# Kernel optimization log

Hardware: AMD Instinct MI355X
Metric: run time of the kernel (lower is better)

Reference implementation:

```python
import jax, jax.numpy as jnp
import numpy as np

B, N, D1, D2, H = 1, 1024, 128, 64, 4
C = D1 // H
PQ = PV = 4
DHALF = D2 // 2


def _ln(x, g, b):
    m = jnp.mean(x, -1, keepdims=True)
    v = jnp.var(x, -1, keepdims=True)
    return (x - m) / jnp.sqrt(v + 1e-5) * g + b


def _ipa(x, R, t, wq, wk, wv, wqp, wkp, wvp, headw, wout, bout):
    # AlphaFold2-style Invariant Point Attention (no pair bias: none is passed).
    q = (x @ wq).reshape(B, N, H, C)
    k = (x @ wk).reshape(B, N, H, C)
    v = (x @ wv).reshape(B, N, H, C)
    qp = (x @ wqp).reshape(B, N, H, PQ, 3)
    kp = (x @ wkp).reshape(B, N, H, PQ, 3)
    vp = (x @ wvp).reshape(B, N, H, PV, 3)
    to_glob = lambda p: jnp.einsum('bnij,bnhpj->bnhpi', R, p) + t[:, :, None, None, :]
    qpg, kpg, vpg = to_glob(qp), to_glob(kp), to_glob(vp)
    scalar = jnp.einsum('bihc,bjhc->bhij', q, k) / np.sqrt(C).astype(np.float32)
    # squared point distances via expansion (avoids B,N,N,H,P,3 intermediate)
    qq = jnp.sum(qpg ** 2, axis=(-1, -2))  # (B,N,H)
    kk = jnp.sum(kpg ** 2, axis=(-1, -2))
    qk = jnp.einsum('bihpx,bjhpx->bhij', qpg, kpg)
    d2 = qq.transpose(0, 2, 1)[:, :, :, None] + kk.transpose(0, 2, 1)[:, :, None, :] - 2.0 * qk
    gamma = jax.nn.softplus(headw)  # (H,)
    wC = np.float32(np.sqrt(2.0 / (9.0 * PQ)))
    wL = np.float32(np.sqrt(0.5))  # two logit terms
    logits = wL * (scalar - gamma[None, :, None, None] * (wC * 0.5) * d2)
    att = jax.nn.softmax(logits, axis=-1)  # (B,H,N,N)
    o = jnp.einsum('bhij,bjhc->bihc', att, v).reshape(B, N, H * C)
    opt = jnp.einsum('bhij,bjhpx->bihpx', att, vpg)  # global output points
    opt_l = jnp.einsum('bnji,bnhpj->bnhpi', R, opt - t[:, :, None, None, :])  # back to local frame
    norms = jnp.sqrt(jnp.sum(opt_l ** 2, -1) + 1e-8)  # (B,N,H,PV)
    feat = jnp.concatenate([o, opt_l.reshape(B, N, H * PV * 3), norms.reshape(B, N, H * PV)], -1)
    return feat @ wout + bout


def _forward(seq_1d, pair_2d, frames_R, frames_t,
             ln1_g, ln1_b, w_qkv, b_qkv, w_o, b_o, w_2to1, b_2to1,
             lnff_g, lnff_b, w_ff1, b_ff1, w_ff2, b_ff2,
             w_l, b_l, w_r, b_r, w_conv, b_conv,
             ipa_wq, ipa_wk, ipa_wv, ipa_wqp, ipa_wkp, ipa_wvp,
             ipa_headw, ipa_wout, ipa_bout, ln3_g, ln3_b):
    # --- 1D track: pre-LN MHA ---
    res = seq_1d
    xn = _ln(seq_1d, ln1_g, ln1_b)
    qkv = xn @ w_qkv + b_qkv  # (B,N,3*D1)
    q, k, v = jnp.split(qkv, 3, axis=-1)
    q = q.reshape(B, N, H, C); k = k.reshape(B, N, H, C); v = v.reshape(B, N, H, C)
    att = jax.nn.softmax(jnp.einsum('bihc,bjhc->bhij', q, k) / np.sqrt(C).astype(np.float32), -1)
    a = jnp.einsum('bhij,bjhc->bihc', att, v).reshape(B, N, D1) @ w_o + b_o
    x = res + a  # dropout is identity in eval
    # --- pair -> 1D aggregation (mean over j of INPUT pair) ---
    x = x + pair_2d.mean(axis=2) @ w_2to1 + b_2to1
    # --- FFN ---
    hdn = _ln(x, lnff_g, lnff_b)
    x = x + jax.nn.gelu(hdn @ w_ff1 + b_ff1, approximate=False) @ w_ff2 + b_ff2
    # --- 1D -> pair outer(-sum) update, zero-padded to D2 channels ---
    left = x @ w_l + b_l    # (B,N,D2//2)
    right = x @ w_r + b_r
    outer = left[:, :, None, :] + right[:, None, :, :]  # (B,N,N,D2//2)
    pair = pair_2d + jnp.pad(outer, ((0, 0), (0, 0), (0, 0), (0, D2 - DHALF)))
    # --- 1x1 conv on pair == per-position channel mixing ---
    pair = pair + (pair @ w_conv + b_conv)
    # --- IPA + post-norm residual ---
    ipa_out = _ipa(x, frames_R, frames_t, ipa_wq, ipa_wk, ipa_wv,
                   ipa_wqp, ipa_wkp, ipa_wvp, ipa_headw, ipa_wout, ipa_bout)
    x = x + _ln(ipa_out, ln3_g, ln3_b)
    return x, pair, frames_R, frames_t


def setup_inputs() -> dict:
    key = jax.random.key(0)
    ks = iter(jax.random.split(key, 48))
    nk = lambda: next(ks)
    w = lambda shape: jax.random.normal(nk(), shape, jnp.float32) * 0.02
    seq_1d = jax.random.normal(nk(), (B, N, D1), jnp.float32)
    pair_2d = jax.random.normal(nk(), (B, N, N, D2), jnp.float32)
    frames_R, _ = jnp.linalg.qr(jax.random.normal(nk(), (B, N, 3, 3), jnp.float32))
    frames_t = jax.random.normal(nk(), (B, N, 3), jnp.float32)
    return {
        'seq_1d': seq_1d, 'pair_2d': pair_2d, 'frames_R': frames_R, 'frames_t': frames_t,
        'ln1_g': jnp.ones(D1), 'ln1_b': jnp.zeros(D1),
        'w_qkv': w((D1, 3 * D1)), 'b_qkv': jnp.zeros(3 * D1),
        'w_o': w((D1, D1)), 'b_o': jnp.zeros(D1),
        'w_2to1': w((D2, D1)), 'b_2to1': jnp.zeros(D1),
        'lnff_g': jnp.ones(D1), 'lnff_b': jnp.zeros(D1),
        'w_ff1': w((D1, 4 * D1)), 'b_ff1': jnp.zeros(4 * D1),
        'w_ff2': w((4 * D1, D1)), 'b_ff2': jnp.zeros(D1),
        'w_l': w((D1, DHALF)), 'b_l': jnp.zeros(DHALF),
        'w_r': w((D1, DHALF)), 'b_r': jnp.zeros(DHALF),
        'w_conv': w((D2, D2)), 'b_conv': jnp.zeros(D2),
        'ipa_wq': w((D1, H * C)), 'ipa_wk': w((D1, H * C)), 'ipa_wv': w((D1, H * C)),
        'ipa_wqp': w((D1, H * PQ * 3)), 'ipa_wkp': w((D1, H * PQ * 3)), 'ipa_wvp': w((D1, H * PV * 3)),
        'ipa_headw': jnp.zeros(H),
        'ipa_wout': w((H * (C + PV * 3 + PV), D1)), 'ipa_bout': jnp.zeros(D1),
        'ln3_g': jnp.ones(D1), 'ln3_b': jnp.zeros(D1),
    }


def reference(seq_1d, pair_2d, frames_R, frames_t,
              ln1_g, ln1_b, w_qkv, b_qkv, w_o, b_o, w_2to1, b_2to1,
              lnff_g, lnff_b, w_ff1, b_ff1, w_ff2, b_ff2,
              w_l, b_l, w_r, b_r, w_conv, b_conv,
              ipa_wq, ipa_wk, ipa_wv, ipa_wqp, ipa_wkp, ipa_wvp,
              ipa_headw, ipa_wout, ipa_bout, ln3_g, ln3_b):
    return _forward(seq_1d, pair_2d, frames_R, frames_t,
                    ln1_g, ln1_b, w_qkv, b_qkv, w_o, b_o, w_2to1, b_2to1,
                    lnff_g, lnff_b, w_ff1, b_ff1, w_ff2, b_ff2,
                    w_l, b_l, w_r, b_r, w_conv, b_conv,
                    ipa_wq, ipa_wk, ipa_wv, ipa_wqp, ipa_wkp, ipa_wvp,
                    ipa_headw, ipa_wout, ipa_bout, ln3_g, ln3_b)
```

## Files before the change

kernel.cpp:

```cpp
#include <hip/hip_runtime.h>
#include <math.h>

#define NSEQ 1024
#define D1C 128
#define D2C 64
#define NH 4
#define CH 32

typedef __attribute__((ext_vector_type(8))) short bf16x8;
typedef __attribute__((ext_vector_type(4))) float f32x4;

__device__ __forceinline__ short f2bf(float f) {
    unsigned u = __float_as_uint(f);
    unsigned r = (u + 0x7fffu + ((u >> 16) & 1u)) >> 16;
    return (short)r;
}

__device__ __forceinline__ float block_reduce_sum(float v, float* s) {
    __syncthreads();
    int lane = threadIdx.x & 63, wid = threadIdx.x >> 6;
#pragma unroll
    for (int off = 32; off > 0; off >>= 1) v += __shfl_down(v, off, 64);
    if (lane == 0) s[wid] = v;
    __syncthreads();
    float t = 0.f;
    int nw = (blockDim.x + 63) >> 6;
    for (int w = 0; w < nw; ++w) t += s[w];
    return t;
}

__device__ __forceinline__ float block_reduce_max(float v, float* s) {
    __syncthreads();
    int lane = threadIdx.x & 63, wid = threadIdx.x >> 6;
#pragma unroll
    for (int off = 32; off > 0; off >>= 1) v = fmaxf(v, __shfl_down(v, off, 64));
    if (lane == 0) s[wid] = v;
    __syncthreads();
    float t = -1e30f;
    int nw = (blockDim.x + 63) >> 6;
    for (int w = 0; w < nw; ++w) t = fmaxf(t, s[w]);
    return t;
}

__global__ __launch_bounds__(256) void pair_mean_k(const float* __restrict__ pin,
                                                   float* __restrict__ pmean) {
    int i = blockIdx.x;
    int c4 = threadIdx.x & 15;
    int g  = threadIdx.x >> 4;
    const float4* p4 = (const float4*)(pin + ((size_t)i << 16));
    float4 acc = {0.f, 0.f, 0.f, 0.f};
    for (int j = g; j < NSEQ; j += 16) {
        float4 v = p4[j * 16 + c4];
        acc.x += v.x; acc.y += v.y; acc.z += v.z; acc.w += v.w;
    }
    __shared__ float4 s[256];
    s[threadIdx.x] = acc;
    __syncthreads();
    if (threadIdx.x < 16) {
        float4 t = {0.f, 0.f, 0.f, 0.f};
        for (int gg = 0; gg < 16; ++gg) {
            float4 v = s[gg * 16 + threadIdx.x];
            t.x += v.x; t.y += v.y; t.z += v.z; t.w += v.w;
        }
        const float inv = 1.f / 1024.f;
        t.x *= inv; t.y *= inv; t.z *= inv; t.w *= inv;
        ((float4*)(pmean + i * 64))[threadIdx.x] = t;
    }
}

__global__ __launch_bounds__(128) void ln128_k(const float* __restrict__ x,
                                               const float* __restrict__ g,
                                               const float* __restrict__ b,
                                               const float* __restrict__ res,
                                               float* __restrict__ out) {
    __shared__ float sw[4];
    int i = blockIdx.x, tid = threadIdx.x;
    float v = x[i * D1C + tid];
    float m = block_reduce_sum(v, sw) * (1.f / 128.f);
    float d = v - m;
    float var = block_reduce_sum(d * d, sw) * (1.f / 128.f);
    float y = d * rsqrtf(var + 1e-5f) * g[tid] + b[tid];
    if (res) y += res[i * D1C + tid];
    out[i * D1C + tid] = y;
}

template <int K, int NOUT, int ACT>
__global__ __launch_bounds__(256) void gemm_rows_k(const float* __restrict__ in,
                                                   const float* __restrict__ W,
                                                   const float* __restrict__ bias,
                                                   const float* __restrict__ res,
                                                   float* __restrict__ out) {
    int row0 = blockIdx.x * 4;
    __shared__ float s_in[4][K];
    for (int idx = threadIdx.x; idx < 4 * K; idx += 256) {
        int r = idx / K, k = idx % K;
        s_in[r][k] = in[(row0 + r) * K + k];
    }
    __syncthreads();
    for (int o = threadIdx.x; o < NOUT; o += 256) {
        float a0 = 0.f, a1 = 0.f, a2 = 0.f, a3 = 0.f;
#pragma unroll 4
        for (int k = 0; k < K; ++k) {
            float w = W[k * NOUT + o];
            a0 += s_in[0][k] * w;
            a1 += s_in[1][k] * w;
            a2 += s_in[2][k] * w;
            a3 += s_in[3][k] * w;
        }
        float accs[4] = {a0, a1, a2, a3};
        float bb = bias ? bias[o] : 0.f;
#pragma unroll
        for (int r = 0; r < 4; ++r) {
            float v = accs[r] + bb;
            if (ACT == 1) v = 0.5f * v * (1.f + erff(v * 0.70710678118f));
            if (res) v += res[(row0 + r) * NOUT + o];
            out[(row0 + r) * NOUT + o] = v;
        }
    }
}

__global__ __launch_bounds__(256) void proj_all_k(
    const float* __restrict__ xa,
    const float* __restrict__ wq, const float* __restrict__ wk, const float* __restrict__ wv,
    const float* __restrict__ wqp, const float* __restrict__ wkp, const float* __restrict__ wvp,
    const float* __restrict__ w_l, const float* __restrict__ b_l,
    const float* __restrict__ w_r, const float* __restrict__ b_r,
    float* __restrict__ qb, float* __restrict__ kb, float* __restrict__ vb,
    float* __restrict__ qp, float* __restrict__ kp, float* __restrict__ vp,
    float* __restrict__ left, float* __restrict__ right) {
    int row0 = blockIdx.x * 4;
    __shared__ float s_in[4][128];
    for (int idx = threadIdx.x; idx < 512; idx += 256)
        s_in[idx >> 7][idx & 127] = xa[row0 * 128 + idx];
    __syncthreads();
    for (int o = threadIdx.x; o < 592; o += 256) {
        const float* W; float* dst; int no, oc; float bb = 0.f;
        if (o < 384) {
            int sel = o >> 7; oc = o & 127; no = 128;
            W = sel == 0 ? wq : (sel == 1 ? wk : wv);
            dst = sel == 0 ? qb : (sel == 1 ? kb : vb);
        } else if (o < 528) {
            int r = o - 384; int sel = r / 48; oc = r % 48; no = 48;
            W = sel == 0 ? wqp : (sel == 1 ? wkp : wvp);
            dst = sel == 0 ? qp : (sel == 1 ? kp : vp);
        } else if (o < 560) {
            oc = o - 528; no = 32; W = w_l; dst = left; bb = b_l[oc];
        } else {
            oc = o - 560; no = 32; W = w_r; dst = right; bb = b_r[oc];
        }
        float a0 = 0.f, a1 = 0.f, a2 = 0.f, a3 = 0.f;
#pragma unroll 4
        for (int k = 0; k < 128; ++k) {
            float w = W[k * no + oc];
            a0 += s_in[0][k] * w;
            a1 += s_in[1][k] * w;
            a2 += s_in[2][k] * w;
            a3 += s_in[3][k] * w;
        }
        dst[(row0 + 0) * no + oc] = a0 + bb;
        dst[(row0 + 1) * no + oc] = a1 + bb;
        dst[(row0 + 2) * no + oc] = a2 + bb;
        dst[(row0 + 3) * no + oc] = a3 + bb;
    }
}

__global__ __launch_bounds__(256) void mha_attn_k(const float* __restrict__ qkv,
                                                  float* __restrict__ aout) {
    int i = blockIdx.x >> 2, h = blockIdx.x & 3;
    __shared__ float s_q[32];
    __shared__ float s_p[NSEQ];
    __shared__ float s_r[256];
    __shared__ float sw[8];
    int tid = threadIdx.x;
    if (tid < 32) s_q[tid] = qkv[i * 384 + h * 32 + tid];
    __syncthreads();
    float lv[4];
    float lmax = -1e30f;
#pragma unroll
    for (int it = 0; it < 4; ++it) {
        int j = tid + it * 256;
        const float4* kj = (const float4*)(qkv + j * 384 + 128 + h * 32);
        float dot = 0.f;
#pragma unroll
        for (int c4 = 0; c4 < 8; ++c4) {
            float4 kvv = kj[c4];
            dot += s_q[c4 * 4 + 0] * kvv.x + s_q[c4 * 4 + 1] * kvv.y +
                   s_q[c4 * 4 + 2] * kvv.z + s_q[c4 * 4 + 3] * kvv.w;
        }
        float l = dot * 0.17677669529f;
        lv[it] = l;
        lmax = fmaxf(lmax, l);
    }
    lmax = block_reduce_max(lmax, sw);
    float lsum = 0.f;
#pragma unroll
    for (int it = 0; it < 4; ++it) {
        float e = __expf(lv[it] - lmax);
        s_p[tid + it * 256] = e;
        lsum += e;
    }
    lsum = block_reduce_sum(lsum, sw);
    float inv = 1.f / lsum;
    int c = tid & 31, g = tid >> 5;
    float acc = 0.f;
    const float* vbase = qkv + 256 + h * 32 + c;
    for (int j = g * 128; j < g * 128 + 128; ++j) acc += s_p[j] * vbase[j * 384];
    s_r[tid] = acc;
    __syncthreads();
    if (tid < 32) {
        float s = 0.f;
#pragma unroll
        for (int gg = 0; gg < 8; ++gg) s += s_r[gg * 32 + tid];
        aout[i * 128 + h * 32 + tid] = s * inv;
    }
}

__global__ __launch_bounds__(256) void pair_update_mfma_k(
    const float* __restrict__ pin,
    const float* __restrict__ left,
    const float* __restrict__ right,
    const float* __restrict__ wconv,
    const float* __restrict__ bconv,
    float* __restrict__ pout) {
    int i = blockIdx.x;
    int tid = threadIdx.x;
    int w = tid >> 6;
    int l = tid & 63;
    int lrow = l & 15;
    int kgrp = l >> 4;
    int koff = kgrp * 8;

    bf16x8 Bf[2][4];
#pragma unroll
    for (int kh = 0; kh < 2; ++kh)
#pragma unroll
        for (int nb = 0; nb < 4; ++nb) {
            int col = nb * 16 + lrow;
            bf16x8 bf;
#pragma unroll
            for (int e = 0; e < 8; ++e)
                bf[e] = f2bf(wconv[(kh * 32 + koff + e) * 64 + col]);
            Bf[kh][nb] = bf;
        }
    float lfA[8];
    {
        float4 l0 = *(const float4*)(left + i * 32 + koff);
        float4 l1 = *(const float4*)(left + i * 32 + koff + 4);
        lfA[0] = l0.x; lfA[1] = l0.y; lfA[2] = l0.z; lfA[3] = l0.w;
        lfA[4] = l1.x; lfA[5] = l1.y; lfA[6] = l1.z; lfA[7] = l1.w;
    }
    float biasc[4], leftc[4];
    int cols[4];
#pragma unroll
    for (int nb = 0; nb < 4; ++nb) {
        int col = nb * 16 + lrow;
        cols[nb] = col;
        biasc[nb] = bconv[col];
        leftc[nb] = (col < 32) ? left[i * 32 + col] : 0.f;
    }
    const float* prow = pin + ((size_t)i << 16);
    float* orow = pout + ((size_t)i << 16);

    for (int s = 0; s < 16; ++s) {
        int j0 = s * 64 + w * 16;
        int arow = j0 + lrow;
        const float* pr = prow + arow * 64;
        float4 p0 = *(const float4*)(pr + koff);
        float4 p1 = *(const float4*)(pr + koff + 4);
        float4 r0 = *(const float4*)(right + arow * 32 + koff);
        float4 r1 = *(const float4*)(right + arow * 32 + koff + 4);
        float4 p2 = *(const float4*)(pr + 32 + koff);
        float4 p3 = *(const float4*)(pr + 32 + koff + 4);
        bf16x8 A0, A1;
        A0[0] = f2bf(p0.x + lfA[0] + r0.x);
        A0[1] = f2bf(p0.y + lfA[1] + r0.y);
        A0[2] = f2bf(p0.z + lfA[2] + r0.z);
        A0[3] = f2bf(p0.w + lfA[3] + r0.w);
        A0[4] = f2bf(p1.x + lfA[4] + r1.x);
        A0[5] = f2bf(p1.y + lfA[5] + r1.y);
        A0[6] = f2bf(p1.z + lfA[6] + r1.z);
        A0[7] = f2bf(p1.w + lfA[7] + r1.w);
        A1[0] = f2bf(p2.x); A1[1] = f2bf(p2.y); A1[2] = f2bf(p2.z); A1[3] = f2bf(p2.w);
        A1[4] = f2bf(p3.x); A1[5] = f2bf(p3.y); A1[6] = f2bf(p3.z); A1[7] = f2bf(p3.w);

        f32x4 acc[4];
#pragma unroll
        for (int nb = 0; nb < 4; ++nb) {
            acc[nb] = (f32x4){0.f, 0.f, 0.f, 0.f};
            acc[nb] = __builtin_amdgcn_mfma_f32_16x16x32_bf16(A0, Bf[0][nb], acc[nb], 0, 0, 0);
            acc[nb] = __builtin_amdgcn_mfma_f32_16x16x32_bf16(A1, Bf[1][nb], acc[nb], 0, 0, 0);
        }
        int rbase = j0 + kgrp * 4;
#pragma unroll
        for (int nb = 0; nb < 4; ++nb) {
            int col = cols[nb];
#pragma unroll
            for (int q = 0; q < 4; ++q) {
                int row = rbase + q;
                float p = prow[row * 64 + col];
                float pprime = p + ((col < 32) ? (leftc[nb] + right[row * 32 + col]) : 0.f);
                orow[row * 64 + col] = pprime + acc[nb][q] + biasc[nb];
            }
        }
    }
}

__global__ __launch_bounds__(256) void to_global_k(const float* __restrict__ qp,
                                                   const float* __restrict__ kp,
                                                   const float* __restrict__ vp,
                                                   const float* __restrict__ R,
                                                   const float* __restrict__ t,
                                                   float* __restrict__ qpg,
                                                   float* __restrict__ kpg,
                                                   float* __restrict__ vpg,
                                                   float* __restrict__ qq,
                                                   float* __restrict__ kk) {
    int i = blockIdx.x, tid = threadIdx.x;
    __shared__ float sR[9], sT[3], sG[96];
    if (tid < 9) sR[tid] = R[i * 9 + tid];
    if (tid < 3) sT[tid] = t[i * 3 + tid];
    __syncthreads();
    if (tid < 144) {
        int tensor = tid / 48, rem = tid % 48;
        int comp = rem % 3, base = rem - comp;
        const float* in = (tensor == 0) ? qp : ((tensor == 1) ? kp : vp);
        float v = sT[comp];
#pragma unroll
        for (int jj = 0; jj < 3; ++jj) v += sR[comp * 3 + jj] * in[i * 48 + base + jj];
        float* outp = (tensor == 0) ? qpg : ((tensor == 1) ? kpg : vpg);
        outp[i * 48 + rem] = v;
        if (tensor < 2) sG[tensor * 48 + rem] = v;
    }
    __syncthreads();
    if (tid < 8) {
        int tensor = tid >> 2, h = tid & 3;
        float s = 0.f;
#pragma unroll
        for (int e = 0; e < 12; ++e) {
            float v = sG[tensor * 48 + h * 12 + e];
            s += v * v;
        }
        (tensor == 0 ? qq : kk)[i * 4 + h] = s;
    }
}

__global__ __launch_bounds__(256) void ipa_attn_k(const float* __restrict__ q,
                                                  const float* __restrict__ k,
                                                  const float* __restrict__ v,
                                                  const float* __restrict__ qpg,
                                                  const float* __restrict__ kpg,
                                                  const float* __restrict__ vpg,
                                                  const float* __restrict__ qq,
                                                  const float* __restrict__ kk,
                                                  const float* __restrict__ headw,
                                                  float* __restrict__ feat,
                                                  float* __restrict__ optg) {
    int i = blockIdx.x >> 2, h = blockIdx.x & 3;
    __shared__ float s_q[32], s_qp[12], s_p[NSEQ], s_r[256], sw[8], s_sc[2];
    int tid = threadIdx.x;
    if (tid < 32) s_q[tid] = q[i * 128 + h * 32 + tid];
    if (tid < 12) s_qp[tid] = qpg[i * 48 + h * 12 + tid];
    if (tid == 0) {
        s_sc[0] = qq[i * 4 + h];
        float gamma = log1pf(__expf(headw[h]));
        s_sc[1] = gamma * 0.23570226039f * 0.5f;
    }
    __syncthreads();
    float qqv = s_sc[0], coef = s_sc[1];
    float lv[4];
    float lmax = -1e30f;
#pragma unroll
    for (int it = 0; it < 4; ++it) {
        int j = tid + it * 256;
        const float4* kj = (const float4*)(k + j * 128 + h * 32);
        float dot = 0.f;
#pragma unroll
        for (int c4 = 0; c4 < 8; ++c4) {
            float4 kvv = kj[c4];
            dot += s_q[c4 * 4 + 0] * kvv.x + s_q[c4 * 4 + 1] * kvv.y +
                   s_q[c4 * 4 + 2] * kvv.z + s_q[c4 * 4 + 3] * kvv.w;
        }
        float scalar = dot * 0.17677669529f;
        const float* kpj = kpg + j * 48 + h * 12;
        float d12 = 0.f;
#pragma unroll
        for (int e = 0; e < 12; ++e) d12 += s_qp[e] * kpj[e];
        float d2 = qqv + kk[j * 4 + h] - 2.f * d12;
        float l = 0.70710678118f * (scalar - coef * d2);
        lv[it] = l;
        lmax = fmaxf(lmax, l);
    }
    lmax = block_reduce_max(lmax, sw);
    float lsum = 0.f;
#pragma unroll
    for (int it = 0; it < 4; ++it) {
        float e = __expf(lv[it] - lmax);
        s_p[tid + it * 256] = e;
        lsum += e;
    }
    lsum = block_reduce_sum(lsum, sw);
    float inv = 1.f / lsum;
    int c = tid & 31, g = tid >> 5;
    float acc = 0.f;
    const float* vbase = v + h * 32 + c;
    for (int j = g * 128; j < g * 128 + 128; ++j) acc += s_p[j] * vbase[j * 128];
    s_r[tid] = acc;
    __syncthreads();
    if (tid < 32) {
        float s = 0.f;
#pragma unroll
        for (int gg = 0; gg < 8; ++gg) s += s_r[gg * 32 + tid];
        feat[i * 192 + h * 32 + tid] = s * inv;
    }
    __syncthreads();
    int e2 = tid & 15, g2 = tid >> 4;
    float acc2 = 0.f;
    if (e2 < 12) {
        const float* vpb = vpg + h * 12 + e2;
        for (int j = g2 * 64; j < g2 * 64 + 64; ++j) acc2 += s_p[j] * vpb[j * 48];
    }
    s_r[tid] = acc2;
    __syncthreads();
    if (tid < 12) {
        float s = 0.f;
#pragma unroll
        for (int gg = 0; gg < 16; ++gg) s += s_r[gg * 16 + tid];
        optg[i * 48 + h * 12 + tid] = s * inv;
    }
}

__global__ __launch_bounds__(64) void feat_finish_k(const float* __restrict__ optg,
                                                    const float* __restrict__ R,
                                                    const float* __restrict__ t,
                                                    float* __restrict__ feat) {
    int i = blockIdx.x, tid = threadIdx.x;
    __shared__ float sR[9], sT[3], sL[48];
    if (tid < 9) sR[tid] = R[i * 9 + tid];
    if (tid < 3) sT[tid] = t[i * 3 + tid];
    __syncthreads();
    if (tid < 48) {
        int comp = tid % 3, base = tid - comp;
        float v = 0.f;
#pragma unroll
        for (int jj = 0; jj < 3; ++jj)
            v += sR[jj * 3 + comp] * (optg[i * 48 + base + jj] - sT[jj]);
        sL[tid] = v;
        feat[i * 192 + 128 + tid] = v;
    }
    __syncthreads();
    if (tid < 16) {
        float s = 1e-8f;
#pragma unroll
        for (int comp = 0; comp < 3; ++comp) {
            float v = sL[tid * 3 + comp];
            s += v * v;
        }
        feat[i * 192 + 176 + tid] = sqrtf(s);
    }
}

__global__ __launch_bounds__(256) void copy_frames_k(const float* __restrict__ R,
                                                     const float* __restrict__ t,
                                                     float* __restrict__ out) {
    int idx = blockIdx.x * 256 + threadIdx.x;
    if (idx < 9216) out[idx] = R[idx];
    else if (idx < 12288) out[idx] = t[idx - 9216];
}

extern "C" void kernel_launch(void* const* d_in, const int* in_sizes, int n_in,
                              void* d_out, int out_size, void* d_ws, size_t ws_size,
                              hipStream_t stream) {
    const float* seq    = (const float*)d_in[0];
    const float* pair   = (const float*)d_in[1];
    const float* fR     = (const float*)d_in[2];
    const float* ft     = (const float*)d_in[3];
    const float* ln1g   = (const float*)d_in[4];
    const float* ln1b   = (const float*)d_in[5];
    const float* w_qkv  = (const float*)d_in[6];
    const float* b_qkv  = (const float*)d_in[7];
    const float* w_o    = (const float*)d_in[8];
    const float* b_o    = (const float*)d_in[9];
    const float* w_2to1 = (const float*)d_in[10];
    const float* b_2to1 = (const float*)d_in[11];
    const float* lnffg  = (const float*)d_in[12];
    const float* lnffb  = (const float*)d_in[13];
    const float* w_ff1  = (const float*)d_in[14];
    const float* b_ff1  = (const float*)d_in[15];
    const float* w_ff2  = (const float*)d_in[16];
    const float* b_ff2  = (const float*)d_in[17];
    const float* w_l    = (const float*)d_in[18];
    const float* b_l    = (const float*)d_in[19];
    const float* w_r    = (const float*)d_in[20];
    const float* b_r    = (const float*)d_in[21];
    const float* w_conv = (const float*)d_in[22];
    const float* b_conv = (const float*)d_in[23];
    const float* wq     = (const float*)d_in[24];
    const float* wk     = (const float*)d_in[25];
    const float* wv     = (const float*)d_in[26];
    const float* wqp    = (const float*)d_in[27];
    const float* wkp    = (const float*)d_in[28];
    const float* wvp    = (const float*)d_in[29];
    const float* headw  = (const float*)d_in[30];
    const float* wout   = (const float*)d_in[31];
    const float* bout   = (const float*)d_in[32];
    const float* ln3g   = (const float*)d_in[33];
    const float* ln3b   = (const float*)d_in[34];

    float* ws = (float*)d_ws;
    float* xn      = ws; ws += 131072;
    float* qkvb    = ws; ws += 393216;
    float* abuf    = ws; ws += 131072;
    float* x1      = ws; ws += 131072;
    float* x2      = ws; ws += 131072;
    float* hdn     = ws; ws += 131072;
    float* ff1     = ws; ws += 524288;
    float* xa      = ws; ws += 131072;
    float* pmean   = ws; ws += 65536;
    float* left    = ws; ws += 32768;
    float* right   = ws; ws += 32768;
    float* qb      = ws; ws += 131072;
    float* kb      = ws; ws += 131072;
    float* vb      = ws; ws += 131072;
    float* qp      = ws; ws += 49152;
    float* kp      = ws; ws += 49152;
    float* vp      = ws; ws += 49152;
    float* qpg     = ws; ws += 49152;
    float* kpg     = ws; ws += 49152;
    float* vpg     = ws; ws += 49152;
    float* qqb     = ws; ws += 4096;
    float* kkb     = ws; ws += 4096;
    float* feat    = ws; ws += 196608;
    float* optg    = ws; ws += 49152;
    float* ipa_out = ws; ws += 131072;

    float* out_x    = (float*)d_out;
    float* out_pair = out_x + 131072;
    float* out_R    = out_pair + 67108864;
    float* out_t    = out_R + 9216;

    const int N = NSEQ;

    pair_mean_k<<<N, 256, 0, stream>>>(pair, pmean);

    ln128_k<<<N, 128, 0, stream>>>(seq, ln1g, ln1b, nullptr, xn);
    gemm_rows_k<128, 384, 0><<<N / 4, 256, 0, stream>>>(xn, w_qkv, b_qkv, nullptr, qkvb);
    mha_attn_k<<<N * NH, 256, 0, stream>>>(qkvb, abuf);
    gemm_rows_k<128, 128, 0><<<N / 4, 256, 0, stream>>>(abuf, w_o, b_o, seq, x1);

    gemm_rows_k<64, 128, 0><<<N / 4, 256, 0, stream>>>(pmean, w_2to1, b_2to1, x1, x2);

    ln128_k<<<N, 128, 0, stream>>>(x2, lnffg, lnffb, nullptr, hdn);
    gemm_rows_k<128, 512, 1><<<N / 4, 256, 0, stream>>>(hdn, w_ff1, b_ff1, nullptr, ff1);
    gemm_rows_k<512, 128, 0><<<N / 4, 256, 0, stream>>>(ff1, w_ff2, b_ff2, x2, xa);

    proj_all_k<<<N / 4, 256, 0, stream>>>(xa, wq, wk, wv, wqp, wkp, wvp,
                                          w_l, b_l, w_r, b_r,
                                          qb, kb, vb, qp, kp, vp, left, right);

    pair_update_mfma_k<<<N, 256, 0, stream>>>(pair, left, right, w_conv, b_conv, out_pair);

    to_global_k<<<N, 256, 0, stream>>>(qp, kp, vp, fR, ft, qpg, kpg, vpg, qqb, kkb);

    ipa_attn_k<<<N * NH, 256, 0, stream>>>(qb, kb, vb, qpg, kpg, vpg, qqb, kkb, headw,
                                           feat, optg);

    feat_finish_k<<<N, 64, 0, stream>>>(optg, fR, ft, feat);

    gemm_rows_k<192, 128, 0><<<N / 4, 256, 0, stream>>>(feat, wout, bout, nullptr, ipa_out);

    ln128_k<<<N, 128, 0, stream>>>(ipa_out, ln3g, ln3b, xa, out_x);

    copy_frames_k<<<48, 256, 0, stream>>>(fR, ft, out_t - 9216);
}
```

Measured before the change: 1.183 ms.

## Store keys transposed so attention logit loads coalesce across threads

Adds a transpose kernel for the MHA keys and has the IPA projection and to_global kernels write K, key points and key norms in channel-major (transposed) layout. In both attention kernels each thread now computes two adjacent key positions with float2 loads that are contiguous across the wavefront, replacing strided per-row float4 reads. The IPA point-value accumulation loop is also re-strided so threads in a group read interleaved rows. This costs one extra small kernel launch and some extra workspace writes.

```diff
diff --git a/kernel.cpp b/kernel.cpp
--- a/kernel.cpp
+++ b/kernel.cpp
@@ -119,6 +119,19 @@
     }
 }
 
+template <int LD, int OFF>
+__global__ __launch_bounds__(256) void transposeK_k(const float* __restrict__ in,
+                                                    float* __restrict__ out) {
+    __shared__ float tile[32][33];
+    int jt = blockIdx.x * 32, ct = blockIdx.y * 32;
+    int c = threadIdx.x & 31, r = threadIdx.x >> 5;
+    for (int rr = r; rr < 32; rr += 8)
+        tile[rr][c] = in[(size_t)(jt + rr) * LD + OFF + ct + c];
+    __syncthreads();
+    for (int rr = r; rr < 32; rr += 8)
+        out[(size_t)(ct + rr) * NSEQ + jt + c] = tile[c][rr];
+}
+
 __global__ __launch_bounds__(256) void proj_all_k(
     const float* __restrict__ xa,
     const float* __restrict__ wq, const float* __restrict__ wk, const float* __restrict__ wv,
@@ -127,18 +140,20 @@
     const float* __restrict__ w_r, const float* __restrict__ b_r,
     float* __restrict__ qb, float* __restrict__ kb, float* __restrict__ vb,
     float* __restrict__ qp, float* __restrict__ kp, float* __restrict__ vp,
-    float* __restrict__ left, float* __restrict__ right) {
+    float* __restrict__ left, float* __restrict__ right,
+    float* __restrict__ kTi) {
     int row0 = blockIdx.x * 4;
     __shared__ float s_in[4][128];
     for (int idx = threadIdx.x; idx < 512; idx += 256)
         s_in[idx >> 7][idx & 127] = xa[row0 * 128 + idx];
     __syncthreads();
     for (int o = threadIdx.x; o < 592; o += 256) {
-        const float* W; float* dst; int no, oc; float bb = 0.f;
+        const float* W; float* dst; int no, oc; float bb = 0.f; int isk = 0;
         if (o < 384) {
             int sel = o >> 7; oc = o & 127; no = 128;
             W = sel == 0 ? wq : (sel == 1 ? wk : wv);
             dst = sel == 0 ? qb : (sel == 1 ? kb : vb);
+            isk = (sel == 1);
         } else if (o < 528) {
             int r = o - 384; int sel = r / 48; oc = r % 48; no = 48;
             W = sel == 0 ? wqp : (sel == 1 ? wkp : wvp);
@@ -161,10 +176,15 @@
         dst[(row0 + 1) * no + oc] = a1 + bb;
         dst[(row0 + 2) * no + oc] = a2 + bb;
         dst[(row0 + 3) * no + oc] = a3 + bb;
+        if (isk) {
+            float4 t = {a0, a1, a2, a3};
+            *(float4*)(kTi + (size_t)oc * NSEQ + row0) = t;
+        }
     }
 }
 
 __global__ __launch_bounds__(256) void mha_attn_k(const float* __restrict__ qkv,
+                                                  const float* __restrict__ kTm,
                                                   float* __restrict__ aout) {
     int i = blockIdx.x >> 2, h = blockIdx.x & 3;
     __shared__ float s_q[32];
@@ -177,27 +197,29 @@
     float lv[4];
     float lmax = -1e30f;
 #pragma unroll
-    for (int it = 0; it < 4; ++it) {
-        int j = tid + it * 256;
-        const float4* kj = (const float4*)(qkv + j * 384 + 128 + h * 32);
-        float dot = 0.f;
-#pragma unroll
-        for (int c4 = 0; c4 < 8; ++c4) {
-            float4 kvv = kj[c4];
-            dot += s_q[c4 * 4 + 0] * kvv.x + s_q[c4 * 4 + 1] * kvv.y +
-                   s_q[c4 * 4 + 2] * kvv.z + s_q[c4 * 4 + 3] * kvv.w;
-        }
-        float l = dot * 0.17677669529f;
-        lv[it] = l;
-        lmax = fmaxf(lmax, l);
+    for (int it = 0; it < 2; ++it) {
+        int j = 2 * tid + it * 512;
+        float d0 = 0.f, d1 = 0.f;
+#pragma unroll
+        for (int c = 0; c < 32; ++c) {
+            float2 kv = *(const float2*)(kTm + (size_t)(h * 32 + c) * NSEQ + j);
+            d0 += s_q[c] * kv.x;
+            d1 += s_q[c] * kv.y;
+        }
+        float l0 = d0 * 0.17677669529f;
+        float l1 = d1 * 0.17677669529f;
+        lv[2 * it] = l0; lv[2 * it + 1] = l1;
+        lmax = fmaxf(lmax, fmaxf(l0, l1));
     }
     lmax = block_reduce_max(lmax, sw);
     float lsum = 0.f;
 #pragma unroll
-    for (int it = 0; it < 4; ++it) {
-        float e = __expf(lv[it] - lmax);
-        s_p[tid + it * 256] = e;
-        lsum += e;
+    for (int it = 0; it < 2; ++it) {
+        int j = 2 * tid + it * 512;
+        float e0 = __expf(lv[2 * it] - lmax);
+        float e1 = __expf(lv[2 * it + 1] - lmax);
+        ((float2*)s_p)[j >> 1] = (float2){e0, e1};
+        lsum += e0 + e1;
     }
     lsum = block_reduce_sum(lsum, sw);
     float inv = 1.f / lsum;
@@ -311,10 +333,10 @@
                                                    const float* __restrict__ R,
                                                    const float* __restrict__ t,
                                                    float* __restrict__ qpg,
-                                                   float* __restrict__ kpg,
+                                                   float* __restrict__ kpgT,
                                                    float* __restrict__ vpg,
                                                    float* __restrict__ qq,
-                                                   float* __restrict__ kk) {
+                                                   float* __restrict__ kkT) {
     int i = blockIdx.x, tid = threadIdx.x;
     __shared__ float sR[9], sT[3], sG[96];
     if (tid < 9) sR[tid] = R[i * 9 + tid];
@@ -327,8 +349,9 @@
         float v = sT[comp];
 #pragma unroll
         for (int jj = 0; jj < 3; ++jj) v += sR[comp * 3 + jj] * in[i * 48 + base + jj];
-        float* outp = (tensor == 0) ? qpg : ((tensor == 1) ? kpg : vpg);
-        outp[i * 48 + rem] = v;
+        if (tensor == 0) qpg[i * 48 + rem] = v;
+        else if (tensor == 1) kpgT[rem * NSEQ + i] = v;
+        else vpg[i * 48 + rem] = v;
         if (tensor < 2) sG[tensor * 48 + rem] = v;
     }
     __syncthreads();
@@ -340,18 +363,19 @@
             float v = sG[tensor * 48 + h * 12 + e];
             s += v * v;
         }
-        (tensor == 0 ? qq : kk)[i * 4 + h] = s;
+        if (tensor == 0) qq[i * 4 + h] = s;
+        else kkT[h * NSEQ + i] = s;
     }
 }
 
 __global__ __launch_bounds__(256) void ipa_attn_k(const float* __restrict__ q,
-                                                  const float* __restrict__ k,
                                                   const float* __restrict__ v,
+                                                  const float* __restrict__ kTi,
+                                                  const float* __restrict__ kpgT,
+                                                  const float* __restrict__ kkT,
                                                   const float* __restrict__ qpg,
-                                                  const float* __restrict__ kpg,
                                                   const float* __restrict__ vpg,
                                                   const float* __restrict__ qq,
-                                                  const float* __restrict__ kk,
                                                   const float* __restrict__ headw,
                                                   float* __restrict__ feat,
                                                   float* __restrict__ optg) {
@@ -370,33 +394,37 @@
     float lv[4];
     float lmax = -1e30f;
 #pragma unroll
-    for (int it = 0; it < 4; ++it) {
-        int j = tid + it * 256;
-        const float4* kj = (const float4*)(k + j * 128 + h * 32);
-        float dot = 0.f;
-#pragma unroll
-        for (int c4 = 0; c4 < 8; ++c4) {
-            float4 kvv = kj[c4];
-            dot += s_q[c4 * 4 + 0] * kvv.x + s_q[c4 * 4 + 1] * kvv.y +
-                   s_q[c4 * 4 + 2] * kvv.z + s_q[c4 * 4 + 3] * kvv.w;
-        }
-        float scalar = dot * 0.17677669529f;
-        const float* kpj = kpg + j * 48 + h * 12;
-        float d12 = 0.f;
-#pragma unroll
-        for (int e = 0; e < 12; ++e) d12 += s_qp[e] * kpj[e];
-        float d2 = qqv + kk[j * 4 + h] - 2.f * d12;
-        float l = 0.70710678118f * (scalar - coef * d2);
-        lv[it] = l;
-        lmax = fmaxf(lmax, l);
+    for (int it = 0; it < 2; ++it) {
+        int j = 2 * tid + it * 512;
+        float d0 = 0.f, d1 = 0.f;
+#pragma unroll
+        for (int c = 0; c < 32; ++c) {
+            float2 kv = *(const float2*)(kTi + (size_t)(h * 32 + c) * NSEQ + j);
+            d0 += s_q[c] * kv.x;
+            d1 += s_q[c] * kv.y;
+        }
+        float p0 = 0.f, p1 = 0.f;
+#pragma unroll
+        for (int e = 0; e < 12; ++e) {
+            float2 kv = *(const float2*)(kpgT + (size_t)(h * 12 + e) * NSEQ + j);
+            p0 += s_qp[e] * kv.x;
+            p1 += s_qp[e] * kv.y;
+        }
+        float2 kkv = *(const float2*)(kkT + (size_t)h * NSEQ + j);
+        float l0 = 0.70710678118f * (d0 * 0.17677669529f - coef * (qqv + kkv.x - 2.f * p0));
+        float l1 = 0.70710678118f * (d1 * 0.17677669529f - coef * (qqv + kkv.y - 2.f * p1));
+        lv[2 * it] = l0; lv[2 * it + 1] = l1;
+        lmax = fmaxf(lmax, fmaxf(l0, l1));
     }
     lmax = block_reduce_max(lmax, sw);
     float lsum = 0.f;
 #pragma unroll
-    for (int it = 0; it < 4; ++it) {
-        float e = __expf(lv[it] - lmax);
-        s_p[tid + it * 256] = e;
-        lsum += e;
+    for (int it = 0; it < 2; ++it) {
+        int j = 2 * tid + it * 512;
+        float e0 = __expf(lv[2 * it] - lmax);
+        float e1 = __expf(lv[2 * it + 1] - lmax);
+        ((float2*)s_p)[j >> 1] = (float2){e0, e1};
+        lsum += e0 + e1;
     }
     lsum = block_reduce_sum(lsum, sw);
     float inv = 1.f / lsum;
@@ -417,7 +445,10 @@
     float acc2 = 0.f;
     if (e2 < 12) {
         const float* vpb = vpg + h * 12 + e2;
-        for (int j = g2 * 64; j < g2 * 64 + 64; ++j) acc2 += s_p[j] * vpb[j * 48];
+        for (int jj = 0; jj < 64; ++jj) {
+            int j = g2 + (jj << 4);
+            acc2 += s_p[j] * vpb[j * 48];
+        }
     }
     s_r[tid] = acc2;
     __syncthreads();
@@ -525,13 +556,15 @@
     float* kp      = ws; ws += 49152;
     float* vp      = ws; ws += 49152;
     float* qpg     = ws; ws += 49152;
-    float* kpg     = ws; ws += 49152;
     float* vpg     = ws; ws += 49152;
     float* qqb     = ws; ws += 4096;
-    float* kkb     = ws; ws += 4096;
     float* feat    = ws; ws += 196608;
     float* optg    = ws; ws += 49152;
     float* ipa_out = ws; ws += 131072;
+    float* kTm     = ws; ws += 131072;
+    float* kTi     = ws; ws += 131072;
+    float* kpgT    = ws; ws += 49152;
+    float* kkT     = ws; ws += 4096;
 
     float* out_x    = (float*)d_out;
     float* out_pair = out_x + 131072;
@@ -544,7 +577,8 @@
 
     ln128_k<<<N, 128, 0, stream>>>(seq, ln1g, ln1b, nullptr, xn);
     gemm_rows_k<128, 384, 0><<<N / 4, 256, 0, stream>>>(xn, w_qkv, b_qkv, nullptr, qkvb);
-    mha_attn_k<<<N * NH, 256, 0, stream>>>(qkvb, abuf);
+    transposeK_k<384, 128><<<dim3(32, 4), 256, 0, stream>>>(qkvb, kTm);
+    mha_attn_k<<<N * NH, 256, 0, stream>>>(qkvb, kTm, abuf);
     gemm_rows_k<128, 128, 0><<<N / 4, 256, 0, stream>>>(abuf, w_o, b_o, seq, x1);
 
     gemm_rows_k<64, 128, 0><<<N / 4, 256, 0, stream>>>(pmean, w_2to1, b_2to1, x1, x2);
@@ -555,13 +589,13 @@
 
     proj_all_k<<<N / 4, 256, 0, stream>>>(xa, wq, wk, wv, wqp, wkp, wvp,
                                           w_l, b_l, w_r, b_r,
-                                          qb, kb, vb, qp, kp, vp, left, right);
+                                          qb, kb, vb, qp, kp, vp, left, right, kTi);
 
     pair_update_mfma_k<<<N, 256, 0, stream>>>(pair, left, right, w_conv, b_conv, out_pair);
 
-    to_global_k<<<N, 256, 0, stream>>>(qp, kp, vp, fR, ft, qpg, kpg, vpg, qqb, kkb);
-
-    ipa_attn_k<<<N * NH, 256, 0, stream>>>(qb, kb, vb, qpg, kpg, vpg, qqb, kkb, headw,
+    to_global_k<<<N, 256, 0, stream>>>(qp, kp, vp, fR, ft, qpg, kpgT, vpg, qqb, kkT);
+
+    ipa_attn_k<<<N * NH, 256, 0, stream>>>(qb, vb, kTi, kpgT, kkT, qpg, vpg, qqb, headw,
                                            feat, optg);
 
     feat_finish_k<<<N, 64, 0, stream>>>(optg, fR, ft, feat);
```

After: 1.050 ms. 11.3% less time.
